# Kernel optimization log

Measured on AMD Instinct MI355X. Metric: run time of the kernel, lower is better.

The kernel has to match this reference:

```python
import jax, jax.numpy as jnp
import numpy as np

K = 5  # kernel_size per pseudo dim (degree-1 open B-spline)


def spline_conv(x, src, dst, edge_attr, W, root, bias, num_nodes):
    """PyG SplineConv: degree-1 open B-spline, dim=2, kernel_size=5, aggr='mean',
    root weight + bias. W: [K*K, in, out], root: [in, out], bias: [out]."""
    v = edge_attr * (K - 1)                      # [E,2] in [0, K-1]
    k = jnp.clip(jnp.floor(v), 0, K - 2)         # [E,2] lower knot per dim
    frac = v - k                                  # [E,2]
    ki = k.astype(jnp.int32)
    # per-dim linear basis and knot indices for the 2 support points
    b = jnp.stack([1.0 - frac, frac], axis=-1)    # [E,2,2] (dim, s)
    idx = ki[..., None] + jnp.arange(2, dtype=jnp.int32)  # [E,2,2]
    # tensor-product over the 2 pseudo dims -> 4 basis/weight-index pairs per edge
    basis = (b[:, 0, :, None] * b[:, 1, None, :]).reshape(-1, 4)        # [E,4]
    wi = (idx[:, 0, :, None] + K * idx[:, 1, None, :]).reshape(-1, 4)   # [E,4]
    # precompute x @ W_k for all 25 kernels, then gather per edge
    XW = jnp.einsum('ni,kio->nko', x, W)          # [N,25,out]
    msg = jnp.einsum('es,eso->eo', basis, XW[src[:, None], wi])  # [E,out]
    agg = jax.ops.segment_sum(msg, dst, num_segments=num_nodes)  # [N,out]
    deg = jax.ops.segment_sum(jnp.ones_like(dst, dtype=x.dtype), dst,
                              num_segments=num_nodes)
    agg = agg / jnp.maximum(deg, 1.0)[:, None]    # mean aggregation
    return agg + x @ root + bias


def setup_inputs() -> dict:
    key = jax.random.key(0)
    ks = jax.random.split(key, 16)
    N, E = 100000, 1600000
    x = jax.random.normal(ks[0], (N, 2), dtype=jnp.float32)
    edge_index = jax.random.randint(ks[1], (2, E), 0, N, dtype=jnp.int32)
    edge_attr = jax.random.uniform(ks[2], (E, 2), dtype=jnp.float32)
    def glorot(k, shape):
        fan = shape[-2] + shape[-1]
        return jax.random.uniform(k, shape, jnp.float32,
                                  -np.sqrt(6.0 / fan), np.sqrt(6.0 / fan))
    W1 = glorot(ks[3], (25, 2, 16));  root1 = glorot(ks[4], (2, 16))
    W2 = glorot(ks[5], (25, 16, 16)); root2 = glorot(ks[6], (16, 16))
    W3 = glorot(ks[7], (25, 16, 16)); root3 = glorot(ks[8], (16, 16))
    b1 = jnp.zeros((16,), jnp.float32)
    b2 = jnp.zeros((16,), jnp.float32)
    b3 = jnp.zeros((16,), jnp.float32)
    fc_w = glorot(ks[9], (16, 1))
    fc_b = jnp.zeros((1,), jnp.float32)
    return {"x": x, "edge_index": edge_index, "edge_attr": edge_attr,
            "W1": W1, "root1": root1, "b1": b1,
            "W2": W2, "root2": root2, "b2": b2,
            "W3": W3, "root3": root3, "b3": b3,
            "fc_w": fc_w, "fc_b": fc_b}


def reference(x, edge_index, edge_attr, W1, root1, b1, W2, root2, b2,
              W3, root3, b3, fc_w, fc_b):
    N = x.shape[0]
    src, dst = edge_index[0], edge_index[1]
    h = jax.nn.relu(spline_conv(x, src, dst, edge_attr, W1, root1, b1, N))
    h = jax.nn.relu(spline_conv(h, src, dst, edge_attr, W2, root2, b2, N))
    h = jax.nn.relu(spline_conv(h, src, dst, edge_attr, W3, root3, b3, N))
    logits = (h @ fc_w + fc_b).squeeze(-1)        # [N]
    return jax.nn.sigmoid(logits)
```

## Files before the change

kernel.cpp:

```cpp
#include <hip/hip_runtime.h>
#include <math.h>


#define KS 5
#define BW 512
#define TILE 4096

typedef _Float16 h2f __attribute__((ext_vector_type(2)));

__device__ __forceinline__ h2f u2h(unsigned u) { return __builtin_bit_cast(h2f, u); }

#if __has_builtin(__builtin_amdgcn_fdot2)
__device__ __forceinline__ float fdot2(h2f a, h2f b, float c) {
    return __builtin_amdgcn_fdot2(a, b, c, false);
}
#else
__device__ __forceinline__ float fdot2(h2f a, h2f b, float c) {
    return c + (float)a[0] * (float)b[0] + (float)a[1] * (float)b[1];
}
#endif

__device__ __forceinline__ unsigned packh2(float lo, float hi) {
    return (unsigned)__builtin_bit_cast(ushort, (_Float16)lo) |
           ((unsigned)__builtin_bit_cast(ushort, (_Float16)hi) << 16);
}

__global__ void bucket_hist_kernel(const int* __restrict__ dst, int* __restrict__ bcnt,
                                   int E, int B) {
    __shared__ int lh[256];
    lh[threadIdx.x] = 0;
    __syncthreads();
    int stride = gridDim.x * blockDim.x;
    for (int e = blockIdx.x * blockDim.x + threadIdx.x; e < E; e += stride)
        atomicAdd(&lh[dst[e] >> 9], 1);
    __syncthreads();
    int c = lh[threadIdx.x];
    if ((int)threadIdx.x < B && c) atomicAdd(&bcnt[threadIdx.x], c);
}

__global__ void bucket_scan_kernel(const int* __restrict__ bcnt, int* __restrict__ bbase,
                                   int* __restrict__ bcursor, int B, int E) {
    __shared__ int sh[256];
    int v = ((int)threadIdx.x < B) ? bcnt[threadIdx.x] : 0;
    sh[threadIdx.x] = v;
    __syncthreads();
    for (int off = 1; off < 256; off <<= 1) {
        int t = (threadIdx.x >= (unsigned)off) ? sh[threadIdx.x - off] : 0;
        __syncthreads();
        sh[threadIdx.x] += t;
        __syncthreads();
    }
    if ((int)threadIdx.x < B) {
        bbase[threadIdx.x] = sh[threadIdx.x] - v;
        bcursor[threadIdx.x] = 0;
    }
    if (threadIdx.x == 0) bbase[B] = E;
}

__global__ __launch_bounds__(256) void bin_kernel(
        const float* __restrict__ eattr, const int* __restrict__ src,
        const int* __restrict__ dst, const int* __restrict__ bbase,
        int* __restrict__ bcursor, uint2* __restrict__ bin, int E) {
    __shared__ int lh[256];
    __shared__ int labs[256];
    __shared__ int lcur[256];
    lh[threadIdx.x] = 0;
    lcur[threadIdx.x] = 0;
    __syncthreads();
    int t0 = blockIdx.x * TILE;
    #pragma unroll
    for (int it = 0; it < TILE / 256; ++it) {
        int e = t0 + it * 256 + threadIdx.x;
        if (e < E) atomicAdd(&lh[dst[e] >> 9], 1);
    }
    __syncthreads();
    {
        int c = lh[threadIdx.x];
        if (c) labs[threadIdx.x] = bbase[threadIdx.x] + atomicAdd(&bcursor[threadIdx.x], c);
    }
    __syncthreads();
    #pragma unroll
    for (int it = 0; it < TILE / 256; ++it) {
        int e = t0 + it * 256 + threadIdx.x;
        if (e < E) {
            float2 ea = reinterpret_cast<const float2*>(eattr)[e];
            float a0 = ea.x * (float)(KS - 1);
            float a1 = ea.y * (float)(KS - 1);
            float k0 = fminf(fmaxf(floorf(a0), 0.0f), (float)(KS - 2));
            float k1 = fminf(fmaxf(floorf(a1), 0.0f), (float)(KS - 2));
            float f0 = a0 - k0, f1 = a1 - k1;
            unsigned w00 = (unsigned)((int)k0 + KS * (int)k1);
            int d = dst[e];
            int b = d >> 9;
            unsigned dloc = (unsigned)(d & 511);
            unsigned w0 = (unsigned)src[e] | ((dloc & 255u) << 17) | (w00 << 25) |
                          ((dloc >> 8) << 30);
            int p = atomicAdd(&lcur[b], 1);
            bin[labs[b] + p] = make_uint2(w0, packh2(f0, f1));
        }
    }
}

__global__ __launch_bounds__(256) void bucket_scatter_kernel(
        const uint2* __restrict__ bin, const int* __restrict__ bbase,
        uint2* __restrict__ epack, int* __restrict__ offs, int N, int E) {
    __shared__ int lcnt[512];
    __shared__ int loff[512];
    __shared__ int lcur[512];
    __shared__ int ssc[256];
    int tid = threadIdx.x;
    int b = blockIdx.x;
    int base = bbase[b];
    int cntb = bbase[b + 1] - base;
    int nbase = b << 9;
    lcnt[tid] = 0; lcnt[tid + 256] = 0;
    lcur[tid] = 0; lcur[tid + 256] = 0;
    __syncthreads();
    for (int r = tid; r < cntb; r += 256) {
        unsigned w0 = bin[base + r].x;
        int dloc = (int)(((w0 >> 17) & 255u) | (((w0 >> 30) & 1u) << 8));
        atomicAdd(&lcnt[dloc], 1);
    }
    __syncthreads();
    int a0 = lcnt[2 * tid], a1 = lcnt[2 * tid + 1];
    ssc[tid] = a0 + a1;
    __syncthreads();
    for (int off = 1; off < 256; off <<= 1) {
        int t = (tid >= off) ? ssc[tid - off] : 0;
        __syncthreads();
        ssc[tid] += t;
        __syncthreads();
    }
    int ex = (tid > 0) ? ssc[tid - 1] : 0;
    loff[2 * tid] = ex;
    loff[2 * tid + 1] = ex + a0;
    __syncthreads();
    for (int i = tid; i < 512; i += 256) {
        int n = nbase + i;
        if (n < N) offs[n] = base + loff[i];
    }
    if (b == 0 && tid == 0) offs[N] = E;
    for (int r = tid; r < cntb; r += 256) {
        uint2 rec = bin[base + r];
        int dloc = (int)(((rec.x >> 17) & 255u) | (((rec.x >> 30) & 1u) << 8));
        int p = atomicAdd(&lcur[dloc], 1);
        epack[base + loff[dloc] + p] = make_uint2(rec.x & 0x3E01FFFFu, rec.y);
    }
}

__device__ __forceinline__ void decode8(uint2 pk, int& s, float b[4], int wi[4]) {
    s = (int)(pk.x & 0x1FFFFFFu);
    int w00 = (int)(pk.x >> 25);
    wi[0] = w00; wi[1] = w00 + 1; wi[2] = w00 + KS; wi[3] = w00 + KS + 1;
    h2f f = u2h(pk.y);
    float f0 = (float)f[0], f1 = (float)f[1];
    float g0 = 1.0f - f0, g1 = 1.0f - f1;
    b[0] = g0 * g1; b[1] = f0 * g1; b[2] = g0 * f1; b[3] = f0 * f1;
}

__global__ __launch_bounds__(256, 8) void csr2_kernel(
        const float* __restrict__ x,
        const uint2* __restrict__ epack,
        const int* __restrict__ offs,
        const float* __restrict__ W,
        const float* __restrict__ root,
        const float* __restrict__ bias,
        ushort* __restrict__ hout,
        int N) {
    __shared__ float Wl[25 * 32];
    for (int idx = threadIdx.x; idx < 25 * 32; idx += blockDim.x) {
        int k = idx >> 5;
        int r = idx & 31;
        int i = r >> 4;
        int o = r & 15;
        Wl[k * 32 + o * 2 + i] = W[idx];
    }
    __syncthreads();

    int t = blockIdx.x * blockDim.x + threadIdx.x;
    if (t >= N * 16) return;
    int o = t & 15;
    int n = t >> 4;
    int row = offs[n], end = offs[n + 1];

    float acc = 0.0f;
    uint2 pk = epack[(row < end) ? row : 0];
    for (int j = row; j < end; ++j) {
        uint2 cur = pk;
        int jn = j + 1;
        pk = epack[(jn < end) ? jn : j];
        int s;
        float b[4];
        int wi[4];
        decode8(cur, s, b, wi);
        float2 xv = reinterpret_cast<const float2*>(x)[s];
        #pragma unroll
        for (int sp = 0; sp < 4; ++sp) {
            float2 w = *reinterpret_cast<const float2*>(&Wl[wi[sp] * 32 + o * 2]);
            acc += b[sp] * (xv.x * w.x + xv.y * w.y);
        }
    }
    float inv = 1.0f / fmaxf((float)(end - row), 1.0f);
    float2 xn = reinterpret_cast<const float2*>(x)[n];
    acc = acc * inv + xn.x * root[o] + xn.y * root[16 + o] + bias[o];
    hout[t] = __builtin_bit_cast(ushort, (_Float16)fmaxf(acc, 0.0f));
}

__global__ __launch_bounds__(256, 8) void csr16_kernel(
        const ushort* __restrict__ hh,
        const uint2* __restrict__ epack,
        const int* __restrict__ offs,
        const float* __restrict__ W,
        const float* __restrict__ root,
        const float* __restrict__ bias,
        ushort* __restrict__ hout,
        int N) {
    __shared__ unsigned Wl[25 * 192 + 192];
    for (int idx = threadIdx.x; idx < 25 * 128 + 128; idx += blockDim.x) {
        if (idx < 25 * 128) {
            int k = idx >> 7;
            int d = idx & 127;
            int o = d >> 3;
            int j = d & 7;
            int i0 = ((j >> 2) << 3) + ((j & 3) << 1);
            Wl[k * 192 + o * 12 + j] =
                packh2(W[k * 256 + i0 * 16 + o], W[k * 256 + (i0 + 1) * 16 + o]);
        } else {
            int d = idx - 25 * 128;
            int o = d >> 3;
            int j = d & 7;
            int i0 = ((j >> 2) << 3) + ((j & 3) << 1);
            Wl[4800 + o * 12 + j] = packh2(root[i0 * 16 + o], root[(i0 + 1) * 16 + o]);
        }
    }
    __syncthreads();

    int t = blockIdx.x * blockDim.x + threadIdx.x;
    if (t >= N * 16) return;
    int o = t & 15;
    int n = t >> 4;
    int row = offs[n], end = offs[n + 1];
    int s0 = o * 12;

    float acc = 0.0f;
    uint2 pk = epack[(row < end) ? row : 0];
    for (int j = row; j < end; ++j) {
        uint2 cur = pk;
        int jn = j + 1;
        pk = epack[(jn < end) ? jn : j];
        int s;
        float b[4];
        int wi[4];
        decode8(cur, s, b, wi);
        const uint4* hp = reinterpret_cast<const uint4*>(hh + (size_t)s * 16);
        uint4 ha = hp[0], hb = hp[1];
        #pragma unroll
        for (int sp = 0; sp < 4; ++sp) {
            int kb = wi[sp] * 192 + s0;
            uint4 wa = *reinterpret_cast<const uint4*>(&Wl[kb]);
            uint4 wb = *reinterpret_cast<const uint4*>(&Wl[kb + 4]);
            float p = 0.0f;
            p = fdot2(u2h(ha.x), u2h(wa.x), p);
            p = fdot2(u2h(ha.y), u2h(wa.y), p);
            p = fdot2(u2h(ha.z), u2h(wa.z), p);
            p = fdot2(u2h(ha.w), u2h(wa.w), p);
            p = fdot2(u2h(hb.x), u2h(wb.x), p);
            p = fdot2(u2h(hb.y), u2h(wb.y), p);
            p = fdot2(u2h(hb.z), u2h(wb.z), p);
            p = fdot2(u2h(hb.w), u2h(wb.w), p);
            acc = fmaf(b[sp], p, acc);
        }
    }
    float inv = 1.0f / fmaxf((float)(end - row), 1.0f);
    acc *= inv;
    {
        const uint4* hp = reinterpret_cast<const uint4*>(hh + (size_t)n * 16);
        uint4 ha = hp[0], hb = hp[1];
        uint4 ra = *reinterpret_cast<const uint4*>(&Wl[4800 + s0]);
        uint4 rb = *reinterpret_cast<const uint4*>(&Wl[4800 + s0 + 4]);
        float p = 0.0f;
        p = fdot2(u2h(ha.x), u2h(ra.x), p);
        p = fdot2(u2h(ha.y), u2h(ra.y), p);
        p = fdot2(u2h(ha.z), u2h(ra.z), p);
        p = fdot2(u2h(ha.w), u2h(ra.w), p);
        p = fdot2(u2h(hb.x), u2h(rb.x), p);
        p = fdot2(u2h(hb.y), u2h(rb.y), p);
        p = fdot2(u2h(hb.z), u2h(rb.z), p);
        p = fdot2(u2h(hb.w), u2h(rb.w), p);
        acc += p + bias[o];
    }
    hout[t] = __builtin_bit_cast(ushort, (_Float16)fmaxf(acc, 0.0f));
}

__global__ void fc_kernel(const ushort* __restrict__ h,
                          const float* __restrict__ fcw,
                          const float* __restrict__ fcb,
                          float* __restrict__ out, int N) {
    int n = blockIdx.x * blockDim.x + threadIdx.x;
    if (n >= N) return;
    const uint4* hp = reinterpret_cast<const uint4*>(h + (size_t)n * 16);
    uint4 ha = hp[0], hb = hp[1];
    unsigned dw[8] = {ha.x, ha.y, ha.z, ha.w, hb.x, hb.y, hb.z, hb.w};
    float acc = fcb[0];
    #pragma unroll
    for (int j = 0; j < 8; ++j) {
        h2f p = u2h(dw[j]);
        acc += (float)p[0] * fcw[2 * j] + (float)p[1] * fcw[2 * j + 1];
    }
    out[n] = 1.0f / (1.0f + expf(-acc));
}

__global__ void deg_count_kernel(const int* __restrict__ dst, float* __restrict__ deg, int E) {
    int stride = gridDim.x * blockDim.x;
    for (int e = blockIdx.x * blockDim.x + threadIdx.x; e < E; e += stride)
        atomicAdd(&deg[dst[e]], 1.0f);
}
__global__ void deg_inv_kernel(float* __restrict__ deg, int N) {
    int i = blockIdx.x * blockDim.x + threadIdx.x;
    if (i < N) deg[i] = 1.0f / fmaxf(deg[i], 1.0f);
}
__device__ __forceinline__ void compute_basis(const float* eattr, const int* srcp, int e,
                                              int& s, float b[4], int wi[4]) {
    float2 ea = reinterpret_cast<const float2*>(eattr)[e];
    float a0 = ea.x * (float)(KS - 1);
    float a1 = ea.y * (float)(KS - 1);
    float k0 = fminf(fmaxf(floorf(a0), 0.0f), (float)(KS - 2));
    float k1 = fminf(fmaxf(floorf(a1), 0.0f), (float)(KS - 2));
    float f0 = a0 - k0, f1 = a1 - k1;
    int i0 = (int)k0, i1 = (int)k1;
    int w00 = i0 + KS * i1;
    wi[0] = w00; wi[1] = w00 + 1; wi[2] = w00 + KS; wi[3] = w00 + KS + 1;
    float g0 = 1.0f - f0, g1 = 1.0f - f1;
    b[0] = g0 * g1; b[1] = f0 * g1; b[2] = g0 * f1; b[3] = f0 * f1;
    s = srcp[e];
}
__global__ __launch_bounds__(256) void edge16h_fb(
        const ushort* __restrict__ hh, const int* __restrict__ dst,
        const float* __restrict__ eattr, const int* __restrict__ srcp,
        const float* __restrict__ W, float* __restrict__ agg, int E) {
    __shared__ unsigned Wl[25 * 192];
    for (int idx = threadIdx.x; idx < 25 * 128; idx += blockDim.x) {
        int k = idx >> 7;
        int d = idx & 127;
        int o = d >> 3;
        int j = d & 7;
        int i0 = ((j >> 2) << 3) + ((j & 3) << 1);
        Wl[k * 192 + o * 12 + j] =
            packh2(W[k * 256 + i0 * 16 + o], W[k * 256 + (i0 + 1) * 16 + o]);
    }
    __syncthreads();
    int gs = gridDim.x * blockDim.x;
    int total = E * 16;
    for (int t = blockIdx.x * blockDim.x + threadIdx.x; t < total; t += gs) {
        int e = t >> 4;
        int o = t & 15;
        int s;
        float b[4];
        int wi[4];
        compute_basis(eattr, srcp, e, s, b, wi);
        const uint4* hp = reinterpret_cast<const uint4*>(hh + (size_t)s * 16);
        uint4 ha = hp[0], hb = hp[1];
        float acc = 0.0f;
        #pragma unroll
        for (int sp = 0; sp < 4; ++sp) {
            int kb = wi[sp] * 192 + o * 12;
            uint4 wa = *reinterpret_cast<const uint4*>(&Wl[kb]);
            uint4 wb = *reinterpret_cast<const uint4*>(&Wl[kb + 4]);
            float p = 0.0f;
            p = fdot2(u2h(ha.x), u2h(wa.x), p);
            p = fdot2(u2h(ha.y), u2h(wa.y), p);
            p = fdot2(u2h(ha.z), u2h(wa.z), p);
            p = fdot2(u2h(ha.w), u2h(wa.w), p);
            p = fdot2(u2h(hb.x), u2h(wb.x), p);
            p = fdot2(u2h(hb.y), u2h(wb.y), p);
            p = fdot2(u2h(hb.z), u2h(wb.z), p);
            p = fdot2(u2h(hb.w), u2h(wb.w), p);
            acc = fmaf(b[sp], p, acc);
        }
        atomicAdd(&agg[(size_t)dst[e] * 16 + o], acc);
    }
}
__global__ __launch_bounds__(256) void edge2_fb(
        const float* __restrict__ x, const int* __restrict__ dst,
        const float* __restrict__ eattr, const int* __restrict__ srcp,
        const float* __restrict__ W, float* __restrict__ agg, int E) {
    __shared__ float Wl[25 * 32];
    for (int idx = threadIdx.x; idx < 25 * 32; idx += blockDim.x) {
        int k = idx >> 5;
        int r = idx & 31;
        int i = r >> 4;
        int o = r & 15;
        Wl[k * 32 + o * 2 + i] = W[idx];
    }
    __syncthreads();
    int gs = gridDim.x * blockDim.x;
    int total = E * 16;
    for (int t = blockIdx.x * blockDim.x + threadIdx.x; t < total; t += gs) {
        int e = t >> 4;
        int o = t & 15;
        int s;
        float b[4];
        int wi[4];
        compute_basis(eattr, srcp, e, s, b, wi);
        float2 xv = reinterpret_cast<const float2*>(x)[s];
        float acc = 0.0f;
        #pragma unroll
        for (int sp = 0; sp < 4; ++sp) {
            float2 w = *reinterpret_cast<const float2*>(&Wl[wi[sp] * 32 + o * 2]);
            acc += b[sp] * (xv.x * w.x + xv.y * w.y);
        }
        atomicAdd(&agg[(size_t)dst[e] * 16 + o], acc);
    }
}
__global__ void finalize2h_fb(const float* __restrict__ x, const float* __restrict__ root,
                              const float* __restrict__ bias, const float* __restrict__ invdeg,
                              const float* __restrict__ agg, ushort* __restrict__ hout, int N) {
    int t = blockIdx.x * blockDim.x + threadIdx.x;
    if (t >= N * 16) return;
    int o = t & 15;
    int n = t >> 4;
    float2 xv = reinterpret_cast<const float2*>(x)[n];
    float acc = agg[t] * invdeg[n] + xv.x * root[o] + xv.y * root[16 + o] + bias[o];
    hout[t] = __builtin_bit_cast(ushort, (_Float16)fmaxf(acc, 0.0f));
}
__global__ void finalize16h_fb(const ushort* __restrict__ hin, const float* __restrict__ root,
                               const float* __restrict__ bias, const float* __restrict__ invdeg,
                               const float* __restrict__ agg, ushort* __restrict__ hout, int N) {
    int t = blockIdx.x * blockDim.x + threadIdx.x;
    if (t >= N * 16) return;
    int o = t & 15;
    int n = t >> 4;
    const uint4* hp = reinterpret_cast<const uint4*>(hin + (size_t)n * 16);
    uint4 ha = hp[0], hb = hp[1];
    float acc = agg[t] * invdeg[n] + bias[o];
    unsigned dw[8] = {ha.x, ha.y, ha.z, ha.w, hb.x, hb.y, hb.z, hb.w};
    #pragma unroll
    for (int j = 0; j < 8; ++j) {
        h2f p = u2h(dw[j]);
        acc += (float)p[0] * root[(2 * j) * 16 + o] + (float)p[1] * root[(2 * j + 1) * 16 + o];
    }
    hout[t] = __builtin_bit_cast(ushort, (_Float16)fmaxf(acc, 0.0f));
}

extern "C" void kernel_launch(void* const* d_in, const int* in_sizes, int n_in,
                              void* d_out, int out_size, void* d_ws, size_t ws_size,
                              hipStream_t stream) {
    const float* x      = (const float*)d_in[0];
    const int*   eidx   = (const int*)d_in[1];
    const float* eattr  = (const float*)d_in[2];
    const float* W1     = (const float*)d_in[3];
    const float* root1  = (const float*)d_in[4];
    const float* b1     = (const float*)d_in[5];
    const float* W2     = (const float*)d_in[6];
    const float* root2  = (const float*)d_in[7];
    const float* b2     = (const float*)d_in[8];
    const float* W3     = (const float*)d_in[9];
    const float* root3  = (const float*)d_in[10];
    const float* b3     = (const float*)d_in[11];
    const float* fcw    = (const float*)d_in[12];
    const float* fcb    = (const float*)d_in[13];
    float* out = (float*)d_out;

    const int N = in_sizes[0] / 2;
    const int E = in_sizes[2] / 2;
    const int* src = eidx;
    const int* dst = eidx + E;
    const int BT = 256;
    const int B = (N + BW - 1) / BW;

    char* w = (char*)d_ws;
    size_t off = 0;
    uint2* epack = (uint2*)(w + off); off += (size_t)E * 8;
    uint2* bin   = (uint2*)(w + off); off += (size_t)E * 8;
    int* bcnt    = (int*)(w + off);   off += 256 * 4;
    int* bbase   = (int*)(w + off);   off += 257 * 4;
    int* bcursor = (int*)(w + off);   off += 256 * 4;
    int* offs    = (int*)(w + off);   off += ((size_t)N + 1) * 4; off = (off + 15) & ~(size_t)15;
    ushort* hH1  = (ushort*)(w + off); off += (size_t)N * 32;
    ushort* hH2  = (ushort*)(w + off); off += (size_t)N * 32;
    size_t need_csr = off;

    if (ws_size >= need_csr && B <= 256 && N <= (1 << 17)) {
        hipMemsetAsync(bcnt, 0, 256 * 4, stream);
        bucket_hist_kernel<<<1024, BT, 0, stream>>>(dst, bcnt, E, B);
        bucket_scan_kernel<<<1, 256, 0, stream>>>(bcnt, bbase, bcursor, B, E);
        bin_kernel<<<(E + TILE - 1) / TILE, BT, 0, stream>>>(eattr, src, dst, bbase,
                                                             bcursor, bin, E);
        bucket_scatter_kernel<<<B, 256, 0, stream>>>(bin, bbase, epack, offs, N, E);

        int node_grid = (N * 16 + BT - 1) / BT;
        csr2_kernel<<<node_grid, BT, 0, stream>>>(x, epack, offs, W1, root1, b1, hH1, N);
        csr16_kernel<<<node_grid, BT, 0, stream>>>(hH1, epack, offs, W2, root2, b2, hH2, N);
        csr16_kernel<<<node_grid, BT, 0, stream>>>(hH2, epack, offs, W3, root3, b3, hH1, N);
        fc_kernel<<<(N + BT - 1) / BT, BT, 0, stream>>>(hH1, fcw, fcb, out, N);
    } else {
        float* agg = (float*)d_ws;
        float* deg = agg + (size_t)N * 16;
        size_t f17 = ((size_t)N * 17 + 7) & ~(size_t)7;
        ushort* fH1 = (ushort*)((float*)d_ws + f17);
        ushort* fH2 = fH1 + (size_t)N * 16;
        const int EG = 2048;
        int node_grid = (N * 16 + BT - 1) / BT;

        hipMemsetAsync(deg, 0, (size_t)N * 4, stream);
        deg_count_kernel<<<2048, BT, 0, stream>>>(dst, deg, E);
        deg_inv_kernel<<<(N + BT - 1) / BT, BT, 0, stream>>>(deg, N);

        hipMemsetAsync(agg, 0, (size_t)N * 64, stream);
        edge2_fb<<<EG, BT, 0, stream>>>(x, dst, eattr, src, W1, agg, E);
        finalize2h_fb<<<node_grid, BT, 0, stream>>>(x, root1, b1, deg, agg, fH1, N);

        hipMemsetAsync(agg, 0, (size_t)N * 64, stream);
        edge16h_fb<<<EG, BT, 0, stream>>>(fH1, dst, eattr, src, W2, agg, E);
        finalize16h_fb<<<node_grid, BT, 0, stream>>>(fH1, root2, b2, deg, agg, fH2, N);

        hipMemsetAsync(agg, 0, (size_t)N * 64, stream);
        edge16h_fb<<<EG, BT, 0, stream>>>(fH2, dst, eattr, src, W3, agg, E);
        finalize16h_fb<<<node_grid, BT, 0, stream>>>(fH2, root3, b3, deg, agg, fH1, N);

        fc_kernel<<<(N + BT - 1) / BT, BT, 0, stream>>>(fH1, fcw, fcb, out, N);
    }
}
```

Baseline: 314.8 us.

## Degree-sort nodes per bucket and prefetch source features in CSR kernels

Within each 512-node bucket, the scatter kernel now counting-sorts nodes by in-degree into an order array. The CSR layer kernels process nodes in that order, so each wavefront holds nodes of similar degree and idles less on divergent loop lengths. The loops also prefetch the next edge's source features one iteration ahead and split each fdot2 chain into two accumulators for more instruction-level parallelism. The cost is extra shared-memory scans in the scatter kernel, an indirection load per node, and scattered output writes.

```diff
diff --git a/kernel.cpp b/kernel.cpp
--- a/kernel.cpp
+++ b/kernel.cpp
@@ -103,16 +103,19 @@
 
 __global__ __launch_bounds__(256) void bucket_scatter_kernel(
         const uint2* __restrict__ bin, const int* __restrict__ bbase,
-        uint2* __restrict__ epack, int* __restrict__ offs, int N, int E) {
+        uint2* __restrict__ epack, int* __restrict__ offs,
+        int* __restrict__ order, int N, int E) {
     __shared__ int lcnt[512];
     __shared__ int loff[512];
     __shared__ int lcur[512];
     __shared__ int ssc[256];
+    __shared__ int dhist[512];
     int tid = threadIdx.x;
     int b = blockIdx.x;
     int base = bbase[b];
     int cntb = bbase[b + 1] - base;
     int nbase = b << 9;
+    int nvalid = (N - nbase < 512) ? (N - nbase) : 512;
     lcnt[tid] = 0; lcnt[tid + 256] = 0;
     lcur[tid] = 0; lcur[tid + 256] = 0;
     __syncthreads();
@@ -146,22 +149,38 @@
         int p = atomicAdd(&lcur[dloc], 1);
         epack[base + loff[dloc] + p] = make_uint2(rec.x & 0x3E01FFFFu, rec.y);
     }
-}
-
-__device__ __forceinline__ void decode8(uint2 pk, int& s, float b[4], int wi[4]) {
-    s = (int)(pk.x & 0x1FFFFFFu);
-    int w00 = (int)(pk.x >> 25);
-    wi[0] = w00; wi[1] = w00 + 1; wi[2] = w00 + KS; wi[3] = w00 + KS + 1;
-    h2f f = u2h(pk.y);
-    float f0 = (float)f[0], f1 = (float)f[1];
-    float g0 = 1.0f - f0, g1 = 1.0f - f1;
-    b[0] = g0 * g1; b[1] = f0 * g1; b[2] = g0 * f1; b[3] = f0 * f1;
+    dhist[tid] = 0; dhist[tid + 256] = 0;
+    __syncthreads();
+    for (int i = tid; i < 512; i += 256) {
+        if (i < nvalid) atomicAdd(&dhist[(lcnt[i] < 511) ? lcnt[i] : 511], 1);
+    }
+    __syncthreads();
+    int c0 = dhist[2 * tid], c1 = dhist[2 * tid + 1];
+    ssc[tid] = c0 + c1;
+    __syncthreads();
+    for (int off = 1; off < 256; off <<= 1) {
+        int t = (tid >= off) ? ssc[tid - off] : 0;
+        __syncthreads();
+        ssc[tid] += t;
+        __syncthreads();
+    }
+    int dex = (tid > 0) ? ssc[tid - 1] : 0;
+    dhist[2 * tid] = dex;
+    dhist[2 * tid + 1] = dex + c0;
+    __syncthreads();
+    for (int i = tid; i < 512; i += 256) {
+        if (i < nvalid) {
+            int r = atomicAdd(&dhist[(lcnt[i] < 511) ? lcnt[i] : 511], 1);
+            order[nbase + r] = nbase + i;
+        }
+    }
 }
 
 __global__ __launch_bounds__(256, 8) void csr2_kernel(
         const float* __restrict__ x,
         const uint2* __restrict__ epack,
         const int* __restrict__ offs,
+        const int* __restrict__ order,
         const float* __restrict__ W,
         const float* __restrict__ root,
         const float* __restrict__ bias,
@@ -180,36 +199,43 @@
     int t = blockIdx.x * blockDim.x + threadIdx.x;
     if (t >= N * 16) return;
     int o = t & 15;
-    int n = t >> 4;
+    int n = order[t >> 4];
     int row = offs[n], end = offs[n + 1];
 
     float acc = 0.0f;
-    uint2 pk = epack[(row < end) ? row : 0];
-    for (int j = row; j < end; ++j) {
-        uint2 cur = pk;
-        int jn = j + 1;
-        pk = epack[(jn < end) ? jn : j];
-        int s;
-        float b[4];
-        int wi[4];
-        decode8(cur, s, b, wi);
-        float2 xv = reinterpret_cast<const float2*>(x)[s];
-        #pragma unroll
-        for (int sp = 0; sp < 4; ++sp) {
-            float2 w = *reinterpret_cast<const float2*>(&Wl[wi[sp] * 32 + o * 2]);
-            acc += b[sp] * (xv.x * w.x + xv.y * w.y);
+    if (row < end) {
+        uint2 pk = epack[row];
+        float2 xn_pf = reinterpret_cast<const float2*>(x)[pk.x & 0x1FFFFFFu];
+        for (int j = row; j < end; ++j) {
+            uint2 cur = pk;
+            float2 xv = xn_pf;
+            int jn = (j + 1 < end) ? j + 1 : j;
+            pk = epack[jn];
+            xn_pf = reinterpret_cast<const float2*>(x)[pk.x & 0x1FFFFFFu];
+            int w00 = (int)((cur.x >> 25) & 31u);
+            h2f f = u2h(cur.y);
+            float f0 = (float)f[0], f1 = (float)f[1];
+            float g0 = 1.0f - f0, g1 = 1.0f - f1;
+            float bb[4] = {g0 * g1, f0 * g1, g0 * f1, f0 * f1};
+            int wiarr[4] = {w00, w00 + 1, w00 + KS, w00 + KS + 1};
+            #pragma unroll
+            for (int sp = 0; sp < 4; ++sp) {
+                float2 w = *reinterpret_cast<const float2*>(&Wl[wiarr[sp] * 32 + o * 2]);
+                acc += bb[sp] * (xv.x * w.x + xv.y * w.y);
+            }
         }
     }
     float inv = 1.0f / fmaxf((float)(end - row), 1.0f);
     float2 xn = reinterpret_cast<const float2*>(x)[n];
     acc = acc * inv + xn.x * root[o] + xn.y * root[16 + o] + bias[o];
-    hout[t] = __builtin_bit_cast(ushort, (_Float16)fmaxf(acc, 0.0f));
+    hout[(size_t)n * 16 + o] = __builtin_bit_cast(ushort, (_Float16)fmaxf(acc, 0.0f));
 }
 
 __global__ __launch_bounds__(256, 8) void csr16_kernel(
         const ushort* __restrict__ hh,
         const uint2* __restrict__ epack,
         const int* __restrict__ offs,
+        const int* __restrict__ order,
         const float* __restrict__ W,
         const float* __restrict__ root,
         const float* __restrict__ bias,
@@ -238,37 +264,44 @@
     int t = blockIdx.x * blockDim.x + threadIdx.x;
     if (t >= N * 16) return;
     int o = t & 15;
-    int n = t >> 4;
+    int n = order[t >> 4];
     int row = offs[n], end = offs[n + 1];
     int s0 = o * 12;
 
     float acc = 0.0f;
-    uint2 pk = epack[(row < end) ? row : 0];
-    for (int j = row; j < end; ++j) {
-        uint2 cur = pk;
-        int jn = j + 1;
-        pk = epack[(jn < end) ? jn : j];
-        int s;
-        float b[4];
-        int wi[4];
-        decode8(cur, s, b, wi);
-        const uint4* hp = reinterpret_cast<const uint4*>(hh + (size_t)s * 16);
-        uint4 ha = hp[0], hb = hp[1];
-        #pragma unroll
-        for (int sp = 0; sp < 4; ++sp) {
-            int kb = wi[sp] * 192 + s0;
-            uint4 wa = *reinterpret_cast<const uint4*>(&Wl[kb]);
-            uint4 wb = *reinterpret_cast<const uint4*>(&Wl[kb + 4]);
-            float p = 0.0f;
-            p = fdot2(u2h(ha.x), u2h(wa.x), p);
-            p = fdot2(u2h(ha.y), u2h(wa.y), p);
-            p = fdot2(u2h(ha.z), u2h(wa.z), p);
-            p = fdot2(u2h(ha.w), u2h(wa.w), p);
-            p = fdot2(u2h(hb.x), u2h(wb.x), p);
-            p = fdot2(u2h(hb.y), u2h(wb.y), p);
-            p = fdot2(u2h(hb.z), u2h(wb.z), p);
-            p = fdot2(u2h(hb.w), u2h(wb.w), p);
-            acc = fmaf(b[sp], p, acc);
+    if (row < end) {
+        uint2 pk = epack[row];
+        const uint4* hpn = reinterpret_cast<const uint4*>(hh + (size_t)(pk.x & 0x1FFFFFFu) * 16);
+        uint4 ha_n = hpn[0], hb_n = hpn[1];
+        for (int j = row; j < end; ++j) {
+            uint2 cur = pk;
+            uint4 ha = ha_n, hb = hb_n;
+            int jn = (j + 1 < end) ? j + 1 : j;
+            pk = epack[jn];
+            const uint4* hp2 = reinterpret_cast<const uint4*>(hh + (size_t)(pk.x & 0x1FFFFFFu) * 16);
+            ha_n = hp2[0]; hb_n = hp2[1];
+            int w00 = (int)((cur.x >> 25) & 31u);
+            h2f f = u2h(cur.y);
+            float f0 = (float)f[0], f1 = (float)f[1];
+            float g0 = 1.0f - f0, g1 = 1.0f - f1;
+            float bb[4] = {g0 * g1, f0 * g1, g0 * f1, f0 * f1};
+            int wiarr[4] = {w00, w00 + 1, w00 + KS, w00 + KS + 1};
+            #pragma unroll
+            for (int sp = 0; sp < 4; ++sp) {
+                int kb = wiarr[sp] * 192 + s0;
+                uint4 wa = *reinterpret_cast<const uint4*>(&Wl[kb]);
+                uint4 wb = *reinterpret_cast<const uint4*>(&Wl[kb + 4]);
+                float pA = 0.0f, pB = 0.0f;
+                pA = fdot2(u2h(ha.x), u2h(wa.x), pA);
+                pA = fdot2(u2h(ha.y), u2h(wa.y), pA);
+                pA = fdot2(u2h(ha.z), u2h(wa.z), pA);
+                pA = fdot2(u2h(ha.w), u2h(wa.w), pA);
+                pB = fdot2(u2h(hb.x), u2h(wb.x), pB);
+                pB = fdot2(u2h(hb.y), u2h(wb.y), pB);
+                pB = fdot2(u2h(hb.z), u2h(wb.z), pB);
+                pB = fdot2(u2h(hb.w), u2h(wb.w), pB);
+                acc = fmaf(bb[sp], pA + pB, acc);
+            }
         }
     }
     float inv = 1.0f / fmaxf((float)(end - row), 1.0f);
@@ -278,18 +311,18 @@
         uint4 ha = hp[0], hb = hp[1];
         uint4 ra = *reinterpret_cast<const uint4*>(&Wl[4800 + s0]);
         uint4 rb = *reinterpret_cast<const uint4*>(&Wl[4800 + s0 + 4]);
-        float p = 0.0f;
-        p = fdot2(u2h(ha.x), u2h(ra.x), p);
-        p = fdot2(u2h(ha.y), u2h(ra.y), p);
-        p = fdot2(u2h(ha.z), u2h(ra.z), p);
-        p = fdot2(u2h(ha.w), u2h(ra.w), p);
-        p = fdot2(u2h(hb.x), u2h(rb.x), p);
-        p = fdot2(u2h(hb.y), u2h(rb.y), p);
-        p = fdot2(u2h(hb.z), u2h(rb.z), p);
-        p = fdot2(u2h(hb.w), u2h(rb.w), p);
-        acc += p + bias[o];
-    }
-    hout[t] = __builtin_bit_cast(ushort, (_Float16)fmaxf(acc, 0.0f));
+        float pA = 0.0f, pB = 0.0f;
+        pA = fdot2(u2h(ha.x), u2h(ra.x), pA);
+        pA = fdot2(u2h(ha.y), u2h(ra.y), pA);
+        pA = fdot2(u2h(ha.z), u2h(ra.z), pA);
+        pA = fdot2(u2h(ha.w), u2h(ra.w), pA);
+        pB = fdot2(u2h(hb.x), u2h(rb.x), pB);
+        pB = fdot2(u2h(hb.y), u2h(rb.y), pB);
+        pB = fdot2(u2h(hb.z), u2h(rb.z), pB);
+        pB = fdot2(u2h(hb.w), u2h(rb.w), pB);
+        acc += pA + pB + bias[o];
+    }
+    hout[(size_t)n * 16 + o] = __builtin_bit_cast(ushort, (_Float16)fmaxf(acc, 0.0f));
 }
 
 __global__ void fc_kernel(const ushort* __restrict__ h,
@@ -475,7 +508,8 @@
     int* bcnt    = (int*)(w + off);   off += 256 * 4;
     int* bbase   = (int*)(w + off);   off += 257 * 4;
     int* bcursor = (int*)(w + off);   off += 256 * 4;
-    int* offs    = (int*)(w + off);   off += ((size_t)N + 1) * 4; off = (off + 15) & ~(size_t)15;
+    int* offs    = (int*)(w + off);   off += ((size_t)N + 1) * 4;
+    int* order   = (int*)(w + off);   off += (size_t)N * 4; off = (off + 15) & ~(size_t)15;
     ushort* hH1  = (ushort*)(w + off); off += (size_t)N * 32;
     ushort* hH2  = (ushort*)(w + off); off += (size_t)N * 32;
     size_t need_csr = off;
@@ -486,12 +520,12 @@
         bucket_scan_kernel<<<1, 256, 0, stream>>>(bcnt, bbase, bcursor, B, E);
         bin_kernel<<<(E + TILE - 1) / TILE, BT, 0, stream>>>(eattr, src, dst, bbase,
                                                              bcursor, bin, E);
-        bucket_scatter_kernel<<<B, 256, 0, stream>>>(bin, bbase, epack, offs, N, E);
+        bucket_scatter_kernel<<<B, 256, 0, stream>>>(bin, bbase, epack, offs, order, N, E);
 
         int node_grid = (N * 16 + BT - 1) / BT;
-        csr2_kernel<<<node_grid, BT, 0, stream>>>(x, epack, offs, W1, root1, b1, hH1, N);
-        csr16_kernel<<<node_grid, BT, 0, stream>>>(hH1, epack, offs, W2, root2, b2, hH2, N);
-        csr16_kernel<<<node_grid, BT, 0, stream>>>(hH2, epack, offs, W3, root3, b3, hH1, N);
+        csr2_kernel<<<node_grid, BT, 0, stream>>>(x, epack, offs, order, W1, root1, b1, hH1, N);
+        csr16_kernel<<<node_grid, BT, 0, stream>>>(hH1, epack, offs, order, W2, root2, b2, hH2, N);
+        csr16_kernel<<<node_grid, BT, 0, stream>>>(hH2, epack, offs, order, W3, root3, b3, hH1, N);
         fc_kernel<<<(N + BT - 1) / BT, BT, 0, stream>>>(hH1, fcw, fcb, out, N);
     } else {
         float* agg = (float*)d_ws;
```

Result: slower. 367.8 us (+16.8%).
